# Performance work log

Measured on AMD Instinct MI355X. Metric: run time of the kernel, lower is better.

Reference implementation:

```python
import jax, jax.numpy as jnp
import numpy as np
from jax import lax

_DN = ('NCHW', 'OIHW', 'NCHW')


def _box1(s, k):
    # Separable box sum (all-ones kxk kernel) on a single-channel map (B,1,H,W).
    pad = (k - 1) // 2
    kh = jnp.ones((1, 1, k, 1), s.dtype)
    kw = jnp.ones((1, 1, 1, k), s.dtype)
    y = lax.conv_general_dilated(s, kh, (1, 1), [(pad, pad), (0, 0)], dimension_numbers=_DN)
    return lax.conv_general_dilated(y, kw, (1, 1), [(0, 0), (pad, pad)], dimension_numbers=_DN)


def _cgf(x, y, k, eps):
    # ConvGuidedFilterDlicate with weight-1 Conv2d(C,C,k): every output channel of
    # box_filter(t) equals box_sum(t.sum(channels)), so we keep channel dim = 1 and broadcast.
    B, C, H, W = x.shape
    Nc = C * _box1(jnp.ones((1, 1, H, W), x.dtype), k)           # box_filter(ones(1,C,H,W))
    mean_x = _box1(x.sum(1, keepdims=True), k) / Nc              # (B,1,H,W)
    mean_y = _box1(y.sum(1, keepdims=True), k) / Nc
    cov_xy = _box1((x * y).sum(1, keepdims=True), k) / Nc - mean_x * mean_y
    var_x = _box1((x * x).sum(1, keepdims=True), k) / Nc - mean_x * mean_x
    A = cov_xy / (var_x + eps)
    b = mean_y - A * mean_x
    # torch's A/b have C identical channels; box_filter then sums them -> factor C.
    mean_A = C * _box1(A, k)
    mean_b = C * _box1(b, k)
    return mean_A * y + mean_b                                   # broadcasts to (B,C,H,W)


def setup_inputs() -> dict:
    key = jax.random.key(0)
    k1, k2 = jax.random.split(key)
    x_hr = jax.random.normal(k1, (16, 3, 512, 512), jnp.float32)
    w1 = jax.random.normal(k2, (3, 9), jnp.float32) * 0.1        # conv1 weight (O, 3*nin1)
    return {"x_hr": x_hr, "w1": w1}


def reference(x_hr, w1):
    F1 = _cgf(x_hr, x_hr, 3, 0.16)
    F2 = _cgf(F1, F1, 7, 0.04)
    F3 = _cgf(F2, F2, 15, 0.01)
    D = jnp.concatenate([x_hr - F1, F1 - F2, F2 - F3], axis=1)   # (B,9,H,W)
    return jnp.einsum('oi,bihw->bohw', w1, D)                    # 1x1 conv, no bias
```

## Files before the change

kernel.cpp:

```cpp
#include <hip/hip_runtime.h>

#define BB 16
#define HH 512
#define WW 512
#define HWP (HH*WW)
#define NMAP ((size_t)BB*HWP)

struct __align__(16) V4 { float x, y, z, w; };
__device__ __forceinline__ V4 v4(float a, float b, float c, float d) { V4 r; r.x=a; r.y=b; r.z=c; r.w=d; return r; }
__device__ __forceinline__ V4 v4z() { return v4(0.f,0.f,0.f,0.f); }
__device__ __forceinline__ V4 vadd(V4 a, V4 b) { return v4(a.x+b.x, a.y+b.y, a.z+b.z, a.w+b.w); }
__device__ __forceinline__ V4 vsub(V4 a, V4 b) { return v4(a.x-b.x, a.y-b.y, a.z-b.z, a.w-b.w); }

template <int P, int CH, int MODE>
__global__ __launch_bounds__(256, 2)
void stage(const float* __restrict__ xin, const float2* __restrict__ sqin,
           float2* __restrict__ abo, float2* __restrict__ sqo,
           const float2* __restrict__ abp1, const float2* __restrict__ abp2,
           const float* __restrict__ wt, float* __restrict__ outp, float eps)
{
    constexpr int PH  = (P - 1) / 2;
    constexpr int RD  = 2*P + 1;
    constexpr int NIT = CH + 2*P + 1;
    constexpr int NCH = HH / CH;
    constexpr int NWG = BB * NCH;
    constexpr int NPS = 256 + 2*PH;
    constexpr int NEV = 257 + PH;
    constexpr int NOD = 258 + PH;

    __shared__ V4 PS[2][NPS];
    __shared__ V4 EV[2][NEV];
    __shared__ V4 OD[2][NOD];

    const int t  = threadIdx.x;
    int bx = blockIdx.x;
    int bid = (bx & 7) * (NWG / 8) + (bx >> 3);
    const int b  = bid / NCH;
    const int h0 = (bid % NCH) * CH;
    const size_t mb_ = (size_t)b * HWP;
    const float*  xb  = (MODE != 2) ? (xin + (size_t)b * 3 * HWP) : nullptr;
    const float2* sqb = (MODE != 1) ? (sqin + mb_) : nullptr;

    if (t < PH) {
        PS[0][t] = v4z(); PS[1][t] = v4z();
        PS[0][256+PH+t] = v4z(); PS[1][256+PH+t] = v4z();
    }
    if (t < PH + 1) {
        OD[0][t] = v4z(); OD[1][t] = v4z();
        EV[0][256+t] = v4z(); EV[1][256+t] = v4z();
    }

    const int c0 = 2*t, c1 = c0 + 1;
    auto cwf = [&](int c) -> float {
        int lo = c - P < 0 ? 0 : c - P, hi = c + P > WW-1 ? WW-1 : c + P;
        return (float)(hi - lo + 1);
    };
    const float cw0 = cwf(c0), cw1 = cwf(c1);

    auto loadrow = [&](int rr) -> V4 {
        if constexpr (MODE == 1) {
            size_t o = (size_t)rr * WW + c0;
            float2 a0 = *(const float2*)(xb + o);
            float2 a1 = *(const float2*)(xb + o + HWP);
            float2 a2 = *(const float2*)(xb + o + 2*HWP);
            return v4(a0.x+a1.x+a2.x, a0.x*a0.x + a1.x*a1.x + a2.x*a2.x,
                      a0.y+a1.y+a2.y, a0.y*a0.y + a1.y*a1.y + a2.y*a2.y);
        } else {
            float4 v = ((const float4*)(sqb + (size_t)rr * WW))[t];
            return v4(v.x, v.y, v.z, v.w);
        }
    };

    V4 csv = v4z(), cav = v4z();
    V4 rgv[RD];
#pragma unroll
    for (int i = 0; i < RD; ++i) rgv[i] = v4z();

#pragma unroll
    for (int d = 0; d <= 2*P; ++d) {
        int rr = h0 - 2*P + d;
        if (rr >= 0) csv = vadd(csv, loadrow(rr));
    }
    V4 nin = loadrow(h0 + 1);

    float w1r[27];
    if constexpr (MODE == 3) {
#pragma unroll
        for (int k = 0; k < 27; ++k) w1r[k] = wt[k];
    }
    __syncthreads();

#pragma unroll
    for (int j = 0; j < NIT; ++j) {
        const int r  = h0 - P + j;
        const int bf = j & 1;
        V4 e0 = v4(csv.x, csv.y, cav.x, cav.y);
        V4 e1 = v4(csv.z, csv.w, cav.z, cav.w);
        PS[bf][PH + t]     = vadd(e0, e1);
        EV[bf][t]          = e0;
        OD[bf][PH + 1 + t] = e1;

        V4 nin2 = v4z(), outv = v4z();
        if (j < NIT - 2) { int rr = r + 2 + P; if (rr < HH) nin2 = loadrow(rr); }
        if (j < NIT - 1) { int rr = r - P;     if (rr >= 0) outv = loadrow(rr); }
        const int h = r - P - 1;
        V4 dv = v4z();
        float4 q1v = make_float4(0,0,0,0), q2v = make_float4(0,0,0,0);
        float2 xe0 = make_float2(0,0), xe1 = xe0, xe2 = xe0;
        if (j >= 2*P + 1) {
            if constexpr (MODE != 3) {
                dv = loadrow(h);
            } else {
                size_t o = mb_ + (size_t)h * WW + c0;
                q1v = *((const float4*)&abp1[o]);
                q2v = *((const float4*)&abp2[o]);
                size_t xo = (size_t)h * WW + c0;
                xe0 = *(const float2*)(xb + xo);
                xe1 = *(const float2*)(xb + xo + HWP);
                xe2 = *(const float2*)(xb + xo + 2*HWP);
            }
        }
        __syncthreads();

        V4 S = v4z();
#pragma unroll
        for (int i = -PH; i <= PH; ++i) S = vadd(S, PS[bf][PH + t + i]);
        V4 W0 = vadd(S, OD[bf][t]);
        V4 W1 = vadd(S, EV[bf][t + PH + 1]);

        if (j >= 2*P + 1) {
            if constexpr (MODE != 3) {
                size_t o = mb_ + (size_t)h * WW + c0;
                *((float4*)&abo[o]) = make_float4(W0.z, W0.w, W1.z, W1.w);
                float mA0 = 3.f*W0.z, mb0 = 3.f*W0.w;
                float mA1 = 3.f*W1.z, mb1 = 3.f*W1.w;
                *((float4*)&sqo[o]) = make_float4(
                    mA0*dv.x + 3.f*mb0,
                    mA0*mA0*dv.y + 2.f*mA0*mb0*dv.x + 3.f*mb0*mb0,
                    mA1*dv.z + 3.f*mb1,
                    mA1*mA1*dv.w + 2.f*mA1*mb1*dv.z + 3.f*mb1*mb1);
            } else {
                float a3  = 3.f*W0.z, b3  = 3.f*W0.w;
                float a3c = 3.f*W1.z, b3c = 3.f*W1.w;
                float r0[3], r1[3];
#pragma unroll
                for (int c = 0; c < 2; ++c) {
                    float P1 = 3.f * (c ? q1v.z : q1v.x), Q1 = 3.f * (c ? q1v.w : q1v.y);
                    float a2 = 3.f * (c ? q2v.z : q2v.x), b2 = 3.f * (c ? q2v.w : q2v.y);
                    float a3v = c ? a3c : a3,             b3v = c ? b3c : b3;
                    float P2 = a2 * P1,  Q2 = a2 * Q1 + b2;
                    float P3 = a3v * P2, Q3 = a3v * Q2 + b3v;
                    float al[3] = {1.f - P1, P1 - P2, P2 - P3};
                    float be[3] = {-Q1,      Q1 - Q2, Q2 - Q3};
                    float x0 = c ? xe0.y : xe0.x;
                    float x1 = c ? xe1.y : xe1.x;
                    float x2 = c ? xe2.y : xe2.x;
                    float* rr_ = c ? r1 : r0;
#pragma unroll
                    for (int oc = 0; oc < 3; ++oc) {
                        float acc = 0.f;
#pragma unroll
                        for (int gg = 0; gg < 3; ++gg) {
                            float wa = w1r[oc*9 + gg*3 + 0];
                            float wb = w1r[oc*9 + gg*3 + 1];
                            float wc = w1r[oc*9 + gg*3 + 2];
                            acc += al[gg] * (wa*x0 + wb*x1 + wc*x2)
                                 + be[gg] * (wa + wb + wc);
                        }
                        rr_[oc] = acc;
                    }
                }
                float* ob = outp + (size_t)b * 3 * HWP + (size_t)h * WW + c0;
#pragma unroll
                for (int oc = 0; oc < 3; ++oc)
                    *((float2*)(ob + (size_t)oc * HWP)) = make_float2(r0[oc], r1[oc]);
            }
        }

        if (j < NIT - 1) {
            V4 Av = v4z();
            if ((unsigned)r < (unsigned)HH) {
                int lo = r-P < 0 ? 0 : r-P, hi = r+P > HH-1 ? HH-1 : r+P;
                float chh = (float)(hi - lo + 1);
                float rn0 = 1.f/(3.f*chh*cw0), rn1 = 1.f/(3.f*chh*cw1);
                float m0 = W0.x*rn0, m1 = W1.x*rn1;
                float v0 = W0.y*rn0 - m0*m0, v1 = W1.y*rn1 - m1*m1;
                float a0 = v0/(v0 + eps), a1 = v1/(v1 + eps);
                Av = v4(a0, m0*(1.f-a0), a1, m1*(1.f-a1));
            }
            const int ri = j % RD;
            cav = vadd(cav, vsub(Av, rgv[ri]));
            rgv[ri] = Av;
            csv = vadd(csv, vsub(nin, outv));
            nin = nin2;
        }
    }
}

extern "C" void kernel_launch(void* const* d_in, const int* in_sizes, int n_in,
                              void* d_out, int out_size, void* d_ws, size_t ws_size,
                              hipStream_t stream) {
    (void)in_sizes; (void)n_in; (void)out_size; (void)ws_size;
    const float* x  = (const float*)d_in[0];
    const float* w1 = (const float*)d_in[1];
    float* out = (float*)d_out;

    float2* sq1 = (float2*)d_ws;
    float2* sq2 = sq1 + NMAP;
    float2* ab1 = sq2 + NMAP;
    float2* ab2 = ab1 + NMAP;

    dim3 bl(256);

    stage<1,4,1><<<dim3(BB*(HH/4)), bl, 0, stream>>>(x, nullptr, ab1, sq1,
                                        nullptr, nullptr, nullptr, nullptr, 0.16f);
    stage<3,8,2><<<dim3(BB*(HH/8)), bl, 0, stream>>>(nullptr, sq1, ab2, sq2,
                                        nullptr, nullptr, nullptr, nullptr, 0.04f);
    stage<7,8,3><<<dim3(BB*(HH/8)), bl, 0, stream>>>(x, sq2, nullptr, nullptr,
                                        ab1, ab2, w1, out, 0.01f);
}
```

Baseline: 203.8 us.

## Replace LDS horizontal box sums with wave-local shuffles over overlapping column tiles

Each wave now owns a column tile with halo lanes and a row strip, and computes the horizontal box sums with cross-lane shuffles. This replaces the shared-memory exchange and the per-row __syncthreads. Row chunks grow to 16, launch bounds raise occupancy, and the previous-row load is reused instead of reloaded. The cost is redundant halo work and loads, partially masked stores, and weights read from global inside the loop.

```diff
diff --git a/kernel.cpp b/kernel.cpp
--- a/kernel.cpp
+++ b/kernel.cpp
@@ -11,53 +11,59 @@
 __device__ __forceinline__ V4 v4z() { return v4(0.f,0.f,0.f,0.f); }
 __device__ __forceinline__ V4 vadd(V4 a, V4 b) { return v4(a.x+b.x, a.y+b.y, a.z+b.z, a.w+b.w); }
 __device__ __forceinline__ V4 vsub(V4 a, V4 b) { return v4(a.x-b.x, a.y-b.y, a.z-b.z, a.w-b.w); }
+__device__ __forceinline__ V4 shflV4(V4 v, int sl) {
+    V4 r;
+    r.x = __shfl(v.x, sl, 64);
+    r.y = __shfl(v.y, sl, 64);
+    r.z = __shfl(v.z, sl, 64);
+    r.w = __shfl(v.w, sl, 64);
+    return r;
+}
 
 template <int P, int CH, int MODE>
-__global__ __launch_bounds__(256, 2)
+__global__ __launch_bounds__(256, (P == 7) ? 3 : 4)
 void stage(const float* __restrict__ xin, const float2* __restrict__ sqin,
            float2* __restrict__ abo, float2* __restrict__ sqo,
            const float2* __restrict__ abp1, const float2* __restrict__ abp2,
            const float* __restrict__ wt, float* __restrict__ outp, float eps)
 {
     constexpr int PH  = (P - 1) / 2;
+    constexpr int M   = PH + 1;
     constexpr int RD  = 2*P + 1;
+    constexpr int STRIDE = 128 - 8*M;
+    constexpr int NT  = (WW + STRIDE - 1) / STRIDE;
+    constexpr int NST = HH / CH;
     constexpr int NIT = CH + 2*P + 1;
-    constexpr int NCH = HH / CH;
-    constexpr int NWG = BB * NCH;
-    constexpr int NPS = 256 + 2*PH;
-    constexpr int NEV = 257 + PH;
-    constexpr int NOD = 258 + PH;
-
-    __shared__ V4 PS[2][NPS];
-    __shared__ V4 EV[2][NEV];
-    __shared__ V4 OD[2][NOD];
-
-    const int t  = threadIdx.x;
-    int bx = blockIdx.x;
-    int bid = (bx & 7) * (NWG / 8) + (bx >> 3);
-    const int b  = bid / NCH;
-    const int h0 = (bid % NCH) * CH;
+    constexpr int NB  = (BB * NT * NST) / 4;
+
+    const int lane = threadIdx.x & 63;
+    const int bx   = blockIdx.x;
+    const int bid  = (bx & 7) * (NB / 8) + (bx >> 3);
+    const int wid  = bid * 4 + (threadIdx.x >> 6);
+    const int st   = wid % NST;
+    const int ti   = (wid / NST) % NT;
+    const int b    = wid / (NST * NT);
+    const int h0   = st * CH;
+    const int o0   = ti * STRIDE;
+    const int c0   = o0 - 4*M + 2*lane;
+
     const size_t mb_ = (size_t)b * HWP;
     const float*  xb  = (MODE != 2) ? (xin + (size_t)b * 3 * HWP) : nullptr;
     const float2* sqb = (MODE != 1) ? (sqin + mb_) : nullptr;
 
-    if (t < PH) {
-        PS[0][t] = v4z(); PS[1][t] = v4z();
-        PS[0][256+PH+t] = v4z(); PS[1][256+PH+t] = v4z();
-    }
-    if (t < PH + 1) {
-        OD[0][t] = v4z(); OD[1][t] = v4z();
-        EV[0][256+t] = v4z(); EV[1][256+t] = v4z();
-    }
-
-    const int c0 = 2*t, c1 = c0 + 1;
+    const bool cok = (unsigned)c0 < (unsigned)WW;
+    const bool eok = cok && (c0 >= o0) && (c0 < o0 + STRIDE);
+
     auto cwf = [&](int c) -> float {
-        int lo = c - P < 0 ? 0 : c - P, hi = c + P > WW-1 ? WW-1 : c + P;
-        return (float)(hi - lo + 1);
+        int lo = c - P < 0 ? 0 : c - P;
+        int hi = c + P > WW-1 ? WW-1 : c + P;
+        int n  = hi - lo + 1;
+        return (float)(n < 1 ? 1 : n);
     };
-    const float cw0 = cwf(c0), cw1 = cwf(c1);
+    const float cw0 = cwf(c0), cw1 = cwf(c0 + 1);
 
     auto loadrow = [&](int rr) -> V4 {
+        if (!cok || (unsigned)rr >= (unsigned)HH) return v4z();
         if constexpr (MODE == 1) {
             size_t o = (size_t)rr * WW + c0;
             float2 a0 = *(const float2*)(xb + o);
@@ -66,133 +72,122 @@
             return v4(a0.x+a1.x+a2.x, a0.x*a0.x + a1.x*a1.x + a2.x*a2.x,
                       a0.y+a1.y+a2.y, a0.y*a0.y + a1.y*a1.y + a2.y*a2.y);
         } else {
-            float4 v = ((const float4*)(sqb + (size_t)rr * WW))[t];
+            float4 v = *((const float4*)(sqb + (size_t)rr * WW + c0));
             return v4(v.x, v.y, v.z, v.w);
         }
     };
 
-    V4 csv = v4z(), cav = v4z();
+    V4 csv = v4z(), cav = v4z(), prevOut = v4z();
     V4 rgv[RD];
 #pragma unroll
     for (int i = 0; i < RD; ++i) rgv[i] = v4z();
 
 #pragma unroll
-    for (int d = 0; d <= 2*P; ++d) {
-        int rr = h0 - 2*P + d;
-        if (rr >= 0) csv = vadd(csv, loadrow(rr));
-    }
-    V4 nin = loadrow(h0 + 1);
-
-    float w1r[27];
-    if constexpr (MODE == 3) {
-#pragma unroll
-        for (int k = 0; k < 27; ++k) w1r[k] = wt[k];
-    }
-    __syncthreads();
+    for (int d = 0; d <= 2*P; ++d) csv = vadd(csv, loadrow(h0 - 2*P + d));
 
 #pragma unroll
     for (int j = 0; j < NIT; ++j) {
-        const int r  = h0 - P + j;
-        const int bf = j & 1;
-        V4 e0 = v4(csv.x, csv.y, cav.x, cav.y);
-        V4 e1 = v4(csv.z, csv.w, cav.z, cav.w);
-        PS[bf][PH + t]     = vadd(e0, e1);
-        EV[bf][t]          = e0;
-        OD[bf][PH + 1 + t] = e1;
-
-        V4 nin2 = v4z(), outv = v4z();
-        if (j < NIT - 2) { int rr = r + 2 + P; if (rr < HH) nin2 = loadrow(rr); }
-        if (j < NIT - 1) { int rr = r - P;     if (rr >= 0) outv = loadrow(rr); }
+        const int r = h0 - P + j;
         const int h = r - P - 1;
-        V4 dv = v4z();
-        float4 q1v = make_float4(0,0,0,0), q2v = make_float4(0,0,0,0);
-        float2 xe0 = make_float2(0,0), xe1 = xe0, xe2 = xe0;
-        if (j >= 2*P + 1) {
-            if constexpr (MODE != 3) {
-                dv = loadrow(h);
-            } else {
+
+        V4 inv = v4z(), outv = v4z();
+        if (j < NIT - 1) { inv = loadrow(r + 1 + P); outv = loadrow(r - P); }
+
+        float2 q1a = make_float2(0,0), q1b = q1a, q2a = q1a, q2b = q1a;
+        float2 xe0 = q1a, xe1 = q1a, xe2 = q1a;
+        if constexpr (MODE == 3) {
+            if (j >= 2*P + 1 && eok) {
                 size_t o = mb_ + (size_t)h * WW + c0;
-                q1v = *((const float4*)&abp1[o]);
-                q2v = *((const float4*)&abp2[o]);
+                q1a = abp1[o]; q1b = abp1[o + 1];
+                q2a = abp2[o]; q2b = abp2[o + 1];
                 size_t xo = (size_t)h * WW + c0;
                 xe0 = *(const float2*)(xb + xo);
                 xe1 = *(const float2*)(xb + xo + HWP);
                 xe2 = *(const float2*)(xb + xo + 2*HWP);
             }
         }
-        __syncthreads();
-
-        V4 S = v4z();
-#pragma unroll
-        for (int i = -PH; i <= PH; ++i) S = vadd(S, PS[bf][PH + t + i]);
-        V4 W0 = vadd(S, OD[bf][t]);
-        V4 W1 = vadd(S, EV[bf][t + PH + 1]);
+
+        V4 e0 = v4(csv.x, csv.y, cav.x, cav.y);
+        V4 e1 = v4(csv.z, csv.w, cav.z, cav.w);
+        V4 p  = vadd(e0, e1);
+        V4 S  = p;
+#pragma unroll
+        for (int i = 1; i <= PH; ++i)
+            S = vadd(S, vadd(shflV4(p, lane - i), shflV4(p, lane + i)));
+        V4 W0 = vadd(S, shflV4(e1, lane - M));
+        V4 W1 = vadd(S, shflV4(e0, lane + M));
 
         if (j >= 2*P + 1) {
             if constexpr (MODE != 3) {
-                size_t o = mb_ + (size_t)h * WW + c0;
-                *((float4*)&abo[o]) = make_float4(W0.z, W0.w, W1.z, W1.w);
-                float mA0 = 3.f*W0.z, mb0 = 3.f*W0.w;
-                float mA1 = 3.f*W1.z, mb1 = 3.f*W1.w;
-                *((float4*)&sqo[o]) = make_float4(
-                    mA0*dv.x + 3.f*mb0,
-                    mA0*mA0*dv.y + 2.f*mA0*mb0*dv.x + 3.f*mb0*mb0,
-                    mA1*dv.z + 3.f*mb1,
-                    mA1*mA1*dv.w + 2.f*mA1*mb1*dv.z + 3.f*mb1*mb1);
+                if (eok) {
+                    size_t o = mb_ + (size_t)h * WW + c0;
+                    abo[o]     = make_float2(W0.z, W0.w);
+                    abo[o + 1] = make_float2(W1.z, W1.w);
+                    float mA0 = 3.f*W0.z, mb0 = 3.f*W0.w;
+                    float mA1 = 3.f*W1.z, mb1 = 3.f*W1.w;
+                    sqo[o]     = make_float2(mA0*prevOut.x + 3.f*mb0,
+                        mA0*mA0*prevOut.y + 2.f*mA0*mb0*prevOut.x + 3.f*mb0*mb0);
+                    sqo[o + 1] = make_float2(mA1*prevOut.z + 3.f*mb1,
+                        mA1*mA1*prevOut.w + 2.f*mA1*mb1*prevOut.z + 3.f*mb1*mb1);
+                }
             } else {
-                float a3  = 3.f*W0.z, b3  = 3.f*W0.w;
-                float a3c = 3.f*W1.z, b3c = 3.f*W1.w;
-                float r0[3], r1[3];
-#pragma unroll
-                for (int c = 0; c < 2; ++c) {
-                    float P1 = 3.f * (c ? q1v.z : q1v.x), Q1 = 3.f * (c ? q1v.w : q1v.y);
-                    float a2 = 3.f * (c ? q2v.z : q2v.x), b2 = 3.f * (c ? q2v.w : q2v.y);
-                    float a3v = c ? a3c : a3,             b3v = c ? b3c : b3;
-                    float P2 = a2 * P1,  Q2 = a2 * Q1 + b2;
-                    float P3 = a3v * P2, Q3 = a3v * Q2 + b3v;
-                    float al[3] = {1.f - P1, P1 - P2, P2 - P3};
-                    float be[3] = {-Q1,      Q1 - Q2, Q2 - Q3};
-                    float x0 = c ? xe0.y : xe0.x;
-                    float x1 = c ? xe1.y : xe1.x;
-                    float x2 = c ? xe2.y : xe2.x;
-                    float* rr_ = c ? r1 : r0;
-#pragma unroll
-                    for (int oc = 0; oc < 3; ++oc) {
-                        float acc = 0.f;
-#pragma unroll
-                        for (int gg = 0; gg < 3; ++gg) {
-                            float wa = w1r[oc*9 + gg*3 + 0];
-                            float wb = w1r[oc*9 + gg*3 + 1];
-                            float wc = w1r[oc*9 + gg*3 + 2];
-                            acc += al[gg] * (wa*x0 + wb*x1 + wc*x2)
-                                 + be[gg] * (wa + wb + wc);
+                if (eok) {
+                    float a3  = 3.f*W0.z, b3  = 3.f*W0.w;
+                    float a3c = 3.f*W1.z, b3c = 3.f*W1.w;
+                    float r0[3], r1[3];
+#pragma unroll
+                    for (int c = 0; c < 2; ++c) {
+                        float P1 = 3.f * (c ? q1b.x : q1a.x), Q1 = 3.f * (c ? q1b.y : q1a.y);
+                        float a2 = 3.f * (c ? q2b.x : q2a.x), b2 = 3.f * (c ? q2b.y : q2a.y);
+                        float a3v = c ? a3c : a3,             b3v = c ? b3c : b3;
+                        float P2 = a2 * P1,  Q2 = a2 * Q1 + b2;
+                        float P3 = a3v * P2, Q3 = a3v * Q2 + b3v;
+                        float al[3] = {1.f - P1, P1 - P2, P2 - P3};
+                        float be[3] = {-Q1,      Q1 - Q2, Q2 - Q3};
+                        float x0 = c ? xe0.y : xe0.x;
+                        float x1 = c ? xe1.y : xe1.x;
+                        float x2 = c ? xe2.y : xe2.x;
+                        float* rr_ = c ? r1 : r0;
+#pragma unroll
+                        for (int oc = 0; oc < 3; ++oc) {
+                            float acc = 0.f;
+#pragma unroll
+                            for (int gg = 0; gg < 3; ++gg) {
+                                float wa = wt[oc*9 + gg*3 + 0];
+                                float wb = wt[oc*9 + gg*3 + 1];
+                                float wc = wt[oc*9 + gg*3 + 2];
+                                acc += al[gg] * (wa*x0 + wb*x1 + wc*x2)
+                                     + be[gg] * (wa + wb + wc);
+                            }
+                            rr_[oc] = acc;
                         }
-                        rr_[oc] = acc;
                     }
+                    float* ob = outp + (size_t)b * 3 * HWP + (size_t)h * WW + c0;
+#pragma unroll
+                    for (int oc = 0; oc < 3; ++oc)
+                        *((float2*)(ob + (size_t)oc * HWP)) = make_float2(r0[oc], r1[oc]);
                 }
-                float* ob = outp + (size_t)b * 3 * HWP + (size_t)h * WW + c0;
-#pragma unroll
-                for (int oc = 0; oc < 3; ++oc)
-                    *((float2*)(ob + (size_t)oc * HWP)) = make_float2(r0[oc], r1[oc]);
             }
         }
 
         if (j < NIT - 1) {
             V4 Av = v4z();
-            if ((unsigned)r < (unsigned)HH) {
-                int lo = r-P < 0 ? 0 : r-P, hi = r+P > HH-1 ? HH-1 : r+P;
+            if (cok && (unsigned)r < (unsigned)HH) {
+                int lo = r - P < 0 ? 0 : r - P;
+                int hi = r + P > HH-1 ? HH-1 : r + P;
                 float chh = (float)(hi - lo + 1);
-                float rn0 = 1.f/(3.f*chh*cw0), rn1 = 1.f/(3.f*chh*cw1);
-                float m0 = W0.x*rn0, m1 = W1.x*rn1;
-                float v0 = W0.y*rn0 - m0*m0, v1 = W1.y*rn1 - m1*m1;
-                float a0 = v0/(v0 + eps), a1 = v1/(v1 + eps);
-                Av = v4(a0, m0*(1.f-a0), a1, m1*(1.f-a1));
+                float rn0 = 1.f / (3.f * chh * cw0);
+                float rn1 = 1.f / (3.f * chh * cw1);
+                float m0 = W0.x * rn0,         m1 = W1.x * rn1;
+                float v0 = W0.y * rn0 - m0*m0, v1 = W1.y * rn1 - m1*m1;
+                float a0 = v0 / (v0 + eps),    a1 = v1 / (v1 + eps);
+                Av = v4(a0, m0 * (1.f - a0), a1, m1 * (1.f - a1));
             }
             const int ri = j % RD;
             cav = vadd(cav, vsub(Av, rgv[ri]));
             rgv[ri] = Av;
-            csv = vadd(csv, vsub(nin, outv));
-            nin = nin2;
+            csv = vadd(csv, vsub(inv, outv));
+            prevOut = outv;
         }
     }
 }
@@ -211,11 +206,10 @@
     float2* ab2 = ab1 + NMAP;
 
     dim3 bl(256);
-
-    stage<1,4,1><<<dim3(BB*(HH/4)), bl, 0, stream>>>(x, nullptr, ab1, sq1,
+    stage<1,16,1><<<dim3(640), bl, 0, stream>>>(x, nullptr, ab1, sq1,
                                         nullptr, nullptr, nullptr, nullptr, 0.16f);
-    stage<3,8,2><<<dim3(BB*(HH/8)), bl, 0, stream>>>(nullptr, sq1, ab2, sq2,
+    stage<3,16,2><<<dim3(640), bl, 0, stream>>>(nullptr, sq1, ab2, sq2,
                                         nullptr, nullptr, nullptr, nullptr, 0.04f);
-    stage<7,8,3><<<dim3(BB*(HH/8)), bl, 0, stream>>>(x, sq2, nullptr, nullptr,
+    stage<7,16,3><<<dim3(768), bl, 0, stream>>>(x, sq2, nullptr, nullptr,
                                         ab1, ab2, w1, out, 0.01f);
 }
```

Measured after the change: 218.0 us. 7.0% more time.
